# Performance work log

Measured on AMD Instinct MI355X. Metric: run time of the kernel, lower is better.

Reference implementation:

```python
import jax, jax.numpy as jnp
import numpy as np

B, S, D, H = 2, 4096, 768, 12
HD = D // H
SCALE = HD ** -0.5


def setup_inputs() -> dict:
    key = jax.random.key(0)
    k_x, k_wq, k_bq, k_wp, k_bp = jax.random.split(key, 5)
    lim_qkv = (1.0 / D) ** 0.5
    lim_p = (1.0 / D) ** 0.5
    return {
        "x": jax.random.normal(k_x, (B, S, D), dtype=jnp.float32),
        "qkv_w": jax.random.uniform(k_wq, (3 * D, D), dtype=jnp.float32, minval=-lim_qkv, maxval=lim_qkv),
        "qkv_b": jax.random.uniform(k_bq, (3 * D,), dtype=jnp.float32, minval=-lim_qkv, maxval=lim_qkv),
        "proj_w": jax.random.uniform(k_wp, (D, D), dtype=jnp.float32, minval=-lim_p, maxval=lim_p),
        "proj_b": jax.random.uniform(k_bp, (D,), dtype=jnp.float32, minval=-lim_p, maxval=lim_p),
    }


def reference(x, qkv_w, qkv_b, proj_w, proj_b):
    b, s, _ = x.shape
    qkv = x @ qkv_w.T + qkv_b                      # [b, s, 3D]
    q, k, v = jnp.split(qkv, 3, axis=-1)           # each [b, s, D]
    # [b, s, D] -> [b, H, s, HD]
    def to_heads(t):
        return t.reshape(b, s, H, HD).transpose(0, 2, 1, 3)
    q, k, v = to_heads(q), to_heads(k), to_heads(v)
    attn = jnp.einsum("bhqd,bhkd->bhqk", q, k) * SCALE   # [b, H, s, s]
    attn = jax.nn.softmax(attn, axis=-1)
    out = jnp.einsum("bhqk,bhkd->bhqd", attn, v)         # [b, H, s, HD]
    out = out.transpose(0, 2, 1, 3).reshape(b, s, D)
    return out @ proj_w.T + proj_b
```

## Files before the change

### kernel.cpp

```cpp
#include <hip/hip_runtime.h>
#include <hip/hip_bf16.h>


#define B_ 2
#define S_ 4096
#define D_ 768
#define H_ 12
#define HD_ 64
#define TD_ (3 * D_)
#define QKD_ (2 * D_)

static constexpr float LOG2E = 1.4426950408889634f;

typedef __bf16 bf16x8 __attribute__((ext_vector_type(8)));
typedef unsigned short ushortx8 __attribute__((ext_vector_type(8)));
typedef unsigned short ushortx4 __attribute__((ext_vector_type(4)));
typedef float floatx4 __attribute__((ext_vector_type(4)));

__device__ inline unsigned short f2bf(float f) {
  return __builtin_bit_cast(unsigned short, (__bf16)f);
}
__device__ inline float bf2f(unsigned short u) {
  return __uint_as_float(((unsigned int)u) << 16);
}
__device__ inline void glds16(const unsigned short* g, unsigned short* l) {
  __builtin_amdgcn_global_load_lds(
      (const __attribute__((address_space(1))) unsigned int*)g,
      (__attribute__((address_space(3))) unsigned int*)l, 16, 0, 0);
}

__global__ __launch_bounds__(256)
void cvt_bf16(const float* __restrict__ src, unsigned short* __restrict__ dst, int n4) {
  int idx = blockIdx.x * 256 + threadIdx.x;
  if (idx < n4) {
    floatx4 v = *reinterpret_cast<const floatx4*>(&src[(size_t)idx * 4]);
    ushortx4 o;
#pragma unroll
    for (int j = 0; j < 4; ++j) o[j] = f2bf(v[j]);
    *reinterpret_cast<ushortx4*>(&dst[(size_t)idx * 4]) = o;
  }
}

template <int NFR, bool QKV_EPI>
__global__ __launch_bounds__(256)
void gemm_bf16(const unsigned short* __restrict__ A,
               const unsigned short* __restrict__ W,
               const float* __restrict__ bias,
               float* __restrict__ Cf,
               unsigned short* __restrict__ qkbuf,
               unsigned short* __restrict__ vT,
               int M, int N, int K) {
  constexpr int BM = 128, BN = NFR * 32, BK = 64;
  __shared__ __attribute__((aligned(16))) unsigned short As[BM][BK];
  __shared__ __attribute__((aligned(16))) unsigned short Ws[BN][BK];

  const int tid = threadIdx.x;
  const int lane = tid & 63;
  const int wid = tid >> 6;
  const int wm = wid >> 1;
  const int wn = wid & 1;
  const int m0 = blockIdx.y * BM;
  const int n0 = blockIdx.x * BN;
  const int lr = lane & 15;
  const int g = lane >> 4;
  const int e8 = lr & 7;
  const int ro = g * 4;
  const int srow = lane >> 3;
  const int sch = lane & 7;

  floatx4 acc[4][NFR];
#pragma unroll
  for (int m = 0; m < 4; ++m)
#pragma unroll
    for (int n = 0; n < NFR; ++n) acc[m][n] = (floatx4){0.f, 0.f, 0.f, 0.f};

  for (int kb = 0; kb < K; kb += BK) {
#pragma unroll
    for (int c = 0; c < 4; ++c) {
      int seg = wid * 4 + c;
      int row = seg * 8 + srow;
      glds16(&A[(size_t)(m0 + row) * K + kb + ((sch ^ srow) << 3)], &As[seg * 8][0]);
    }
#pragma unroll
    for (int c = 0; c < NFR; ++c) {
      int seg = wid * NFR + c;
      int row = seg * 8 + srow;
      glds16(&W[(size_t)(n0 + row) * K + kb + ((sch ^ srow) << 3)], &Ws[seg * 8][0]);
    }
    __syncthreads();

#pragma unroll
    for (int ks = 0; ks < 2; ++ks) {
      int ch = ((ks << 2) + g) ^ e8;
      bf16x8 af[4], bfr[NFR];
#pragma unroll
      for (int m = 0; m < 4; ++m)
        af[m] = *reinterpret_cast<const bf16x8*>(&As[wm * 64 + m * 16 + lr][ch << 3]);
#pragma unroll
      for (int n = 0; n < NFR; ++n)
        bfr[n] = *reinterpret_cast<const bf16x8*>(&Ws[wn * (NFR * 16) + n * 16 + lr][ch << 3]);
#pragma unroll
      for (int m = 0; m < 4; ++m)
#pragma unroll
        for (int n = 0; n < NFR; ++n)
          acc[m][n] = __builtin_amdgcn_mfma_f32_16x16x32_bf16(af[m], bfr[n], acc[m][n], 0, 0, 0);
    }
    __syncthreads();
  }

#pragma unroll
  for (int n = 0; n < NFR; ++n) {
    int col = n0 + wn * (NFR * 16) + n * 16 + lr;
    float bv = bias[col];
#pragma unroll
    for (int m = 0; m < 4; ++m) {
      int row = m0 + wm * 64 + m * 16 + ro;
      if constexpr (QKV_EPI) {
        if (col >= QKD_) {
          int dcol = col - QKD_;
          int hh = dcol >> 6, dd = dcol & 63;
          int bb = row >> 12, s = row & (S_ - 1);
          int s5 = s & 31;
          int spos = (s & ~31) + ((s5 >> 2) & 3) * 8 + ((s5 >> 4) & 1) * 4;
          ushortx4 o4;
#pragma unroll
          for (int i = 0; i < 4; ++i) o4[i] = f2bf(acc[m][n][i] + bv);
          *reinterpret_cast<ushortx4*>(
              &vT[(size_t)((bb * H_ + hh) * 64 + dd) * S_ + spos]) = o4;
        } else {
#pragma unroll
          for (int i = 0; i < 4; ++i)
            qkbuf[(size_t)(row + i) * QKD_ + col] = f2bf(acc[m][n][i] + bv);
        }
      } else {
#pragma unroll
        for (int i = 0; i < 4; ++i)
          Cf[(size_t)(row + i) * N + col] = acc[m][n][i] + bv;
      }
    }
  }
}

template <int NSPLIT>
__global__ __launch_bounds__(256)
void attn_kernel(const unsigned short* __restrict__ qkbuf,
                 const unsigned short* __restrict__ vT,
                 unsigned short* __restrict__ outb,
                 float* __restrict__ po, float* __restrict__ pl) {
  constexpr int QB = 128, KVB = 64, NT = S_ / KVB / NSPLIT;
  __shared__ __attribute__((aligned(16))) unsigned short L[2 * 8192];

  const int tid = threadIdx.x;
  const int lane = tid & 63;
  const int wid = tid >> 6;
  const int q0 = blockIdx.x * QB;
  const int h = blockIdx.y;
  const int b = (NSPLIT == 1) ? blockIdx.z : (blockIdx.z >> 1);
  const int sp = (NSPLIT == 1) ? 0 : (blockIdx.z & 1);
  const int kvbase = sp * (S_ / NSPLIT);
  const int lr = lane & 15;
  const int g = lane >> 4;
  const int e8 = lr & 7;
  const int wq = wid * 32;

  const unsigned short* Qg = qkbuf + (size_t)b * S_ * QKD_ + (size_t)h * HD_;
  const unsigned short* Kg = Qg + D_;
  const unsigned short* Vg = vT + (size_t)(b * H_ + h) * HD_ * S_;

  const int srow = lane >> 3;
  const int sch = lane & 7;

  bf16x8 qf[2][2];
#pragma unroll
  for (int qt = 0; qt < 2; ++qt)
#pragma unroll
    for (int ks = 0; ks < 2; ++ks) {
      ushortx8 r = *reinterpret_cast<const ushortx8*>(
          &Qg[(size_t)(q0 + wq + qt * 16 + lr) * QKD_ + ks * 32 + g * 8]);
      bf16x8 q;
#pragma unroll
      for (int j = 0; j < 8; ++j) q[j] = (__bf16)(bf2f(r[j]) * (0.125f * LOG2E));
      qf[qt][ks] = q;
    }

  bf16x8 onesf;
#pragma unroll
  for (int j = 0; j < 8; ++j) onesf[j] = (__bf16)1.0f;

  floatx4 lacc[2] = {(floatx4){0.f, 0.f, 0.f, 0.f}, (floatx4){0.f, 0.f, 0.f, 0.f}};
  floatx4 oacc[2][4];
#pragma unroll
  for (int qt = 0; qt < 2; ++qt)
#pragma unroll
    for (int dt = 0; dt < 4; ++dt) oacc[qt][dt] = (floatx4){0.f, 0.f, 0.f, 0.f};

  int koff[4][2], voff[2][4];
#pragma unroll
  for (int kt = 0; kt < 4; ++kt)
#pragma unroll
    for (int ks = 0; ks < 2; ++ks)
      koff[kt][ks] = (kt * 16 + lr) * 64 + ((((ks << 2) + g) ^ e8) << 3);
#pragma unroll
  for (int ks = 0; ks < 2; ++ks)
#pragma unroll
    for (int dt = 0; dt < 4; ++dt)
      voff[ks][dt] = 4096 + (dt * 16 + lr) * 64 + ((((ks << 2) + g) ^ e8) << 3);

  const unsigned short* kp0 = Kg + (size_t)(kvbase + wid * 16 + srow) * QKD_ + ((sch ^ srow) << 3);
  const unsigned short* kp1 = kp0 + (size_t)8 * QKD_;
  const unsigned short* vp0 = Vg + (size_t)(wid * 16 + srow) * S_ + kvbase + ((sch ^ srow) << 3);
  const unsigned short* vp1 = vp0 + (size_t)8 * S_;

#define STAGE(BUF) do { \
    glds16(kp0, &L[(BUF) * 8192 + (wid * 16) * 64]); \
    glds16(kp1, &L[(BUF) * 8192 + (wid * 16 + 8) * 64]); \
    glds16(vp0, &L[(BUF) * 8192 + 4096 + (wid * 16) * 64]); \
    glds16(vp1, &L[(BUF) * 8192 + 4096 + (wid * 16 + 8) * 64]); \
    kp0 += (size_t)KVB * QKD_; kp1 += (size_t)KVB * QKD_; \
    vp0 += KVB; vp1 += KVB; } while (0)

#define COMPUTE(BUF) do { \
    bf16x8 kf[4][2], vf[2][4]; \
    _Pragma("unroll") \
    for (int kt = 0; kt < 4; ++kt) \
      _Pragma("unroll") \
      for (int ks = 0; ks < 2; ++ks) \
        kf[kt][ks] = *reinterpret_cast<const bf16x8*>(&L[(BUF) * 8192 + koff[kt][ks]]); \
    _Pragma("unroll") \
    for (int ks = 0; ks < 2; ++ks) \
      _Pragma("unroll") \
      for (int dt = 0; dt < 4; ++dt) \
        vf[ks][dt] = *reinterpret_cast<const bf16x8*>(&L[(BUF) * 8192 + voff[ks][dt]]); \
    _Pragma("unroll") \
    for (int qt = 0; qt < 2; ++qt) { \
      floatx4 sc[4]; \
      _Pragma("unroll") \
      for (int kt = 0; kt < 4; ++kt) { \
        floatx4 c = (floatx4){0.f, 0.f, 0.f, 0.f}; \
        _Pragma("unroll") \
        for (int ks = 0; ks < 2; ++ks) \
          c = __builtin_amdgcn_mfma_f32_16x16x32_bf16(kf[kt][ks], qf[qt][ks], c, 0, 0, 0); \
        sc[kt] = c; \
      } \
      _Pragma("unroll") \
      for (int kt = 0; kt < 4; ++kt) \
        _Pragma("unroll") \
        for (int i = 0; i < 4; ++i) \
          sc[kt][i] = __builtin_amdgcn_exp2f(sc[kt][i]); \
      bf16x8 pf0, pf1; \
      _Pragma("unroll") \
      for (int j = 0; j < 8; ++j) { \
        pf0[j] = (__bf16)sc[(j >> 2)][j & 3]; \
        pf1[j] = (__bf16)sc[2 + (j >> 2)][j & 3]; \
      } \
      lacc[qt] = __builtin_amdgcn_mfma_f32_16x16x32_bf16(onesf, pf0, lacc[qt], 0, 0, 0); \
      lacc[qt] = __builtin_amdgcn_mfma_f32_16x16x32_bf16(onesf, pf1, lacc[qt], 0, 0, 0); \
      _Pragma("unroll") \
      for (int dt = 0; dt < 4; ++dt) \
        oacc[qt][dt] = __builtin_amdgcn_mfma_f32_16x16x32_bf16(vf[0][dt], pf0, oacc[qt][dt], 0, 0, 0); \
      _Pragma("unroll") \
      for (int dt = 0; dt < 4; ++dt) \
        oacc[qt][dt] = __builtin_amdgcn_mfma_f32_16x16x32_bf16(vf[1][dt], pf1, oacc[qt][dt], 0, 0, 0); \
    } } while (0)

  STAGE(0);
  for (int t = 0; t < NT; t += 2) {
    __syncthreads();
    STAGE(1);
    COMPUTE(0);
    __syncthreads();
    if (t + 2 < NT) STAGE(0);
    COMPUTE(1);
  }
#undef STAGE
#undef COMPUTE

#pragma unroll
  for (int qt = 0; qt < 2; ++qt) {
    float l = lacc[qt][0];
    int q = q0 + wq + qt * 16 + lr;
    if constexpr (NSPLIT == 1) {
      float inv = __builtin_amdgcn_rcpf(l);
      size_t rowbase = ((size_t)b * S_ + q) * D_ + h * HD_;
#pragma unroll
      for (int dt = 0; dt < 4; ++dt) {
        ushortx4 o4;
#pragma unroll
        for (int i = 0; i < 4; ++i) o4[i] = f2bf(oacc[qt][dt][i] * inv);
        *reinterpret_cast<ushortx4*>(&outb[rowbase + dt * 16 + 4 * g]) = o4;
      }
    } else {
      size_t rowbase = ((size_t)(sp * B_ + b) * S_ + q) * D_ + h * HD_;
#pragma unroll
      for (int dt = 0; dt < 4; ++dt)
        *reinterpret_cast<floatx4*>(&po[rowbase + dt * 16 + 4 * g]) = oacc[qt][dt];
      if (lane < 16)
        pl[((size_t)((sp * B_ + b) * H_ + h)) * S_ + q] = l;
    }
  }
}

__global__ __launch_bounds__(256)
void combine_kernel(const float* __restrict__ po, const float* __restrict__ pl,
                    unsigned short* __restrict__ attnbuf) {
  int gid = blockIdx.x * 256 + threadIdx.x;
  int d4 = gid & 15;
  int rest = gid >> 4;
  int h = rest % H_;
  int bq = rest / H_;
  size_t o0 = (size_t)bq * D_ + h * 64 + d4 * 4;
  const size_t half = (size_t)B_ * S_ * D_;
  floatx4 a = *reinterpret_cast<const floatx4*>(&po[o0]);
  floatx4 c = *reinterpret_cast<const floatx4*>(&po[o0 + half]);
  int q = bq & (S_ - 1);
  int b = bq >> 12;
  float l = pl[(size_t)(b * H_ + h) * S_ + q] +
            pl[(size_t)((B_ + b) * H_ + h) * S_ + q];
  float inv = __builtin_amdgcn_rcpf(l);
  ushortx4 o;
#pragma unroll
  for (int i = 0; i < 4; ++i) o[i] = f2bf((a[i] + c[i]) * inv);
  *reinterpret_cast<ushortx4*>(&attnbuf[o0]) = o;
}

extern "C" void kernel_launch(void* const* d_in, const int* in_sizes, int n_in,
                              void* d_out, int out_size, void* d_ws, size_t ws_size,
                              hipStream_t stream) {
  const float* x      = (const float*)d_in[0];
  const float* qkv_w  = (const float*)d_in[1];
  const float* qkv_b  = (const float*)d_in[2];
  const float* proj_w = (const float*)d_in[3];
  const float* proj_b = (const float*)d_in[4];
  float* out = (float*)d_out;

  unsigned short* qkbuf   = (unsigned short*)d_ws;
  unsigned short* vTbuf   = qkbuf + (size_t)B_ * S_ * QKD_;
  unsigned short* attnbuf = vTbuf + (size_t)B_ * H_ * HD_ * S_;
  unsigned short* xbf     = attnbuf + (size_t)B_ * S_ * D_;
  unsigned short* wqkvbf  = xbf + (size_t)B_ * S_ * D_;
  unsigned short* wprojbf = wqkvbf + (size_t)TD_ * D_;
  float* po = (float*)(wprojbf + (size_t)D_ * D_);
  float* pl = po + (size_t)2 * B_ * S_ * D_;

  const size_t need = ((char*)(pl + (size_t)2 * B_ * H_ * S_)) - (char*)d_ws;
  const bool split = ws_size >= need;

  dim3 blk(256);
  cvt_bf16<<<dim3((B_ * S_ * D_ / 4 + 255) / 256), blk, 0, stream>>>(x, xbf, B_ * S_ * D_ / 4);
  cvt_bf16<<<dim3((TD_ * D_ / 4 + 255) / 256), blk, 0, stream>>>(qkv_w, wqkvbf, TD_ * D_ / 4);
  cvt_bf16<<<dim3((D_ * D_ / 4 + 255) / 256), blk, 0, stream>>>(proj_w, wprojbf, D_ * D_ / 4);

  gemm_bf16<4, true><<<dim3(TD_ / 128, (B_ * S_) / 128), blk, 0, stream>>>(
      xbf, wqkvbf, qkv_b, nullptr, qkbuf, vTbuf, B_ * S_, TD_, D_);

  if (split) {
    attn_kernel<2><<<dim3(S_ / 128, H_, B_ * 2), blk, 0, stream>>>(
        qkbuf, vTbuf, attnbuf, po, pl);
    combine_kernel<<<dim3(B_ * S_ * H_ * 16 / 256), blk, 0, stream>>>(po, pl, attnbuf);
  } else {
    attn_kernel<1><<<dim3(S_ / 128, H_, B_), blk, 0, stream>>>(
        qkbuf, vTbuf, attnbuf, nullptr, nullptr);
  }

  gemm_bf16<2, false><<<dim3(D_ / 64, (B_ * S_) / 128), blk, 0, stream>>>(
      attnbuf, wprojbf, proj_b, out, nullptr, nullptr, B_ * S_, D_, D_);
}
```

Baseline: 201.0 us.

## Drop split-KV attention with combine pass, fuse conversions, fold Q scale into GEMM

Removes the two-way KV split in attention and the combine kernel that merged the fp32 partial outputs and row sums. Every block now streams the full KV range and writes normalized bf16 output directly, which avoids the large fp32 partial-result round trip through memory. The cost is half as many attention blocks, so less parallelism to hide latency. It also merges the three fp32-to-bf16 conversion launches into one kernel and applies the softmax scale (times log2 e) to Q in the QKV GEMM epilogue, so the attention kernel no longer rescales Q when loading it.

After: 187.5 us, median of 3. 1.07x faster.

```diff
diff --git a/kernel.cpp b/kernel.cpp
--- a/kernel.cpp
+++ b/kernel.cpp
@@ -11,6 +11,7 @@
 #define QKD_ (2 * D_)
 
 static constexpr float LOG2E = 1.4426950408889634f;
+static constexpr float QSCL = 0.125f * LOG2E;
 
 typedef __bf16 bf16x8 __attribute__((ext_vector_type(8)));
 typedef unsigned short ushortx8 __attribute__((ext_vector_type(8)));
@@ -30,15 +31,20 @@
 }
 
 __global__ __launch_bounds__(256)
-void cvt_bf16(const float* __restrict__ src, unsigned short* __restrict__ dst, int n4) {
+void cvt_all(const float* __restrict__ s0, unsigned short* __restrict__ d0, int n0,
+             const float* __restrict__ s1, unsigned short* __restrict__ d1, int n1,
+             const float* __restrict__ s2, unsigned short* __restrict__ d2, int n2) {
   int idx = blockIdx.x * 256 + threadIdx.x;
-  if (idx < n4) {
-    floatx4 v = *reinterpret_cast<const floatx4*>(&src[(size_t)idx * 4]);
-    ushortx4 o;
-#pragma unroll
-    for (int j = 0; j < 4; ++j) o[j] = f2bf(v[j]);
-    *reinterpret_cast<ushortx4*>(&dst[(size_t)idx * 4]) = o;
-  }
+  const float* s; unsigned short* d;
+  if (idx < n0) { s = s0; d = d0; }
+  else if (idx < n0 + n1) { s = s1; d = d1; idx -= n0; }
+  else if (idx < n0 + n1 + n2) { s = s2; d = d2; idx -= n0 + n1; }
+  else return;
+  floatx4 v = *reinterpret_cast<const floatx4*>(&s[(size_t)idx * 4]);
+  ushortx4 o;
+#pragma unroll
+  for (int j = 0; j < 4; ++j) o[j] = f2bf(v[j]);
+  *reinterpret_cast<ushortx4*>(&d[(size_t)idx * 4]) = o;
 }
 
 template <int NFR, bool QKV_EPI>
@@ -128,9 +134,10 @@
           *reinterpret_cast<ushortx4*>(
               &vT[(size_t)((bb * H_ + hh) * 64 + dd) * S_ + spos]) = o4;
         } else {
+          const float scl = (col < D_) ? QSCL : 1.0f;
 #pragma unroll
           for (int i = 0; i < 4; ++i)
-            qkbuf[(size_t)(row + i) * QKD_ + col] = f2bf(acc[m][n][i] + bv);
+            qkbuf[(size_t)(row + i) * QKD_ + col] = f2bf((acc[m][n][i] + bv) * scl);
         }
       } else {
 #pragma unroll
@@ -141,13 +148,11 @@
   }
 }
 
-template <int NSPLIT>
 __global__ __launch_bounds__(256)
 void attn_kernel(const unsigned short* __restrict__ qkbuf,
                  const unsigned short* __restrict__ vT,
-                 unsigned short* __restrict__ outb,
-                 float* __restrict__ po, float* __restrict__ pl) {
-  constexpr int QB = 128, KVB = 64, NT = S_ / KVB / NSPLIT;
+                 unsigned short* __restrict__ outb) {
+  constexpr int QB = 128, KVB = 64, NT = S_ / KVB;
   __shared__ __attribute__((aligned(16))) unsigned short L[2 * 8192];
 
   const int tid = threadIdx.x;
@@ -155,9 +160,7 @@
   const int wid = tid >> 6;
   const int q0 = blockIdx.x * QB;
   const int h = blockIdx.y;
-  const int b = (NSPLIT == 1) ? blockIdx.z : (blockIdx.z >> 1);
-  const int sp = (NSPLIT == 1) ? 0 : (blockIdx.z & 1);
-  const int kvbase = sp * (S_ / NSPLIT);
+  const int b = blockIdx.z;
   const int lr = lane & 15;
   const int g = lane >> 4;
   const int e8 = lr & 7;
@@ -174,14 +177,9 @@
 #pragma unroll
   for (int qt = 0; qt < 2; ++qt)
 #pragma unroll
-    for (int ks = 0; ks < 2; ++ks) {
-      ushortx8 r = *reinterpret_cast<const ushortx8*>(
+    for (int ks = 0; ks < 2; ++ks)
+      qf[qt][ks] = *reinterpret_cast<const bf16x8*>(
           &Qg[(size_t)(q0 + wq + qt * 16 + lr) * QKD_ + ks * 32 + g * 8]);
-      bf16x8 q;
-#pragma unroll
-      for (int j = 0; j < 8; ++j) q[j] = (__bf16)(bf2f(r[j]) * (0.125f * LOG2E));
-      qf[qt][ks] = q;
-    }
 
   bf16x8 onesf;
 #pragma unroll
@@ -206,9 +204,9 @@
     for (int dt = 0; dt < 4; ++dt)
       voff[ks][dt] = 4096 + (dt * 16 + lr) * 64 + ((((ks << 2) + g) ^ e8) << 3);
 
-  const unsigned short* kp0 = Kg + (size_t)(kvbase + wid * 16 + srow) * QKD_ + ((sch ^ srow) << 3);
+  const unsigned short* kp0 = Kg + (size_t)(wid * 16 + srow) * QKD_ + ((sch ^ srow) << 3);
   const unsigned short* kp1 = kp0 + (size_t)8 * QKD_;
-  const unsigned short* vp0 = Vg + (size_t)(wid * 16 + srow) * S_ + kvbase + ((sch ^ srow) << 3);
+  const unsigned short* vp0 = Vg + (size_t)(wid * 16 + srow) * S_ + ((sch ^ srow) << 3);
   const unsigned short* vp1 = vp0 + (size_t)8 * S_;
 
 #define STAGE(BUF) do { \
@@ -279,48 +277,16 @@
   for (int qt = 0; qt < 2; ++qt) {
     float l = lacc[qt][0];
     int q = q0 + wq + qt * 16 + lr;
-    if constexpr (NSPLIT == 1) {
-      float inv = __builtin_amdgcn_rcpf(l);
-      size_t rowbase = ((size_t)b * S_ + q) * D_ + h * HD_;
-#pragma unroll
-      for (int dt = 0; dt < 4; ++dt) {
-        ushortx4 o4;
-#pragma unroll
-        for (int i = 0; i < 4; ++i) o4[i] = f2bf(oacc[qt][dt][i] * inv);
-        *reinterpret_cast<ushortx4*>(&outb[rowbase + dt * 16 + 4 * g]) = o4;
-      }
-    } else {
-      size_t rowbase = ((size_t)(sp * B_ + b) * S_ + q) * D_ + h * HD_;
-#pragma unroll
-      for (int dt = 0; dt < 4; ++dt)
-        *reinterpret_cast<floatx4*>(&po[rowbase + dt * 16 + 4 * g]) = oacc[qt][dt];
-      if (lane < 16)
-        pl[((size_t)((sp * B_ + b) * H_ + h)) * S_ + q] = l;
+    float inv = __builtin_amdgcn_rcpf(l);
+    size_t rowbase = ((size_t)b * S_ + q) * D_ + h * HD_;
+#pragma unroll
+    for (int dt = 0; dt < 4; ++dt) {
+      ushortx4 o4;
+#pragma unroll
+      for (int i = 0; i < 4; ++i) o4[i] = f2bf(oacc[qt][dt][i] * inv);
+      *reinterpret_cast<ushortx4*>(&outb[rowbase + dt * 16 + 4 * g]) = o4;
     }
   }
-}
-
-__global__ __launch_bounds__(256)
-void combine_kernel(const float* __restrict__ po, const float* __restrict__ pl,
-                    unsigned short* __restrict__ attnbuf) {
-  int gid = blockIdx.x * 256 + threadIdx.x;
-  int d4 = gid & 15;
-  int rest = gid >> 4;
-  int h = rest % H_;
-  int bq = rest / H_;
-  size_t o0 = (size_t)bq * D_ + h * 64 + d4 * 4;
-  const size_t half = (size_t)B_ * S_ * D_;
-  floatx4 a = *reinterpret_cast<const floatx4*>(&po[o0]);
-  floatx4 c = *reinterpret_cast<const floatx4*>(&po[o0 + half]);
-  int q = bq & (S_ - 1);
-  int b = bq >> 12;
-  float l = pl[(size_t)(b * H_ + h) * S_ + q] +
-            pl[(size_t)((B_ + b) * H_ + h) * S_ + q];
-  float inv = __builtin_amdgcn_rcpf(l);
-  ushortx4 o;
-#pragma unroll
-  for (int i = 0; i < 4; ++i) o[i] = f2bf((a[i] + c[i]) * inv);
-  *reinterpret_cast<ushortx4*>(&attnbuf[o0]) = o;
 }
 
 extern "C" void kernel_launch(void* const* d_in, const int* in_sizes, int n_in,
@@ -339,28 +305,16 @@
   unsigned short* xbf     = attnbuf + (size_t)B_ * S_ * D_;
   unsigned short* wqkvbf  = xbf + (size_t)B_ * S_ * D_;
   unsigned short* wprojbf = wqkvbf + (size_t)TD_ * D_;
-  float* po = (float*)(wprojbf + (size_t)D_ * D_);
-  float* pl = po + (size_t)2 * B_ * S_ * D_;
-
-  const size_t need = ((char*)(pl + (size_t)2 * B_ * H_ * S_)) - (char*)d_ws;
-  const bool split = ws_size >= need;
 
   dim3 blk(256);
-  cvt_bf16<<<dim3((B_ * S_ * D_ / 4 + 255) / 256), blk, 0, stream>>>(x, xbf, B_ * S_ * D_ / 4);
-  cvt_bf16<<<dim3((TD_ * D_ / 4 + 255) / 256), blk, 0, stream>>>(qkv_w, wqkvbf, TD_ * D_ / 4);
-  cvt_bf16<<<dim3((D_ * D_ / 4 + 255) / 256), blk, 0, stream>>>(proj_w, wprojbf, D_ * D_ / 4);
+  const int nx = B_ * S_ * D_ / 4, nw1 = TD_ * D_ / 4, nw2 = D_ * D_ / 4;
+  cvt_all<<<dim3((nx + nw1 + nw2 + 255) / 256), blk, 0, stream>>>(
+      x, xbf, nx, qkv_w, wqkvbf, nw1, proj_w, wprojbf, nw2);
 
   gemm_bf16<4, true><<<dim3(TD_ / 128, (B_ * S_) / 128), blk, 0, stream>>>(
       xbf, wqkvbf, qkv_b, nullptr, qkbuf, vTbuf, B_ * S_, TD_, D_);
 
-  if (split) {
-    attn_kernel<2><<<dim3(S_ / 128, H_, B_ * 2), blk, 0, stream>>>(
-        qkbuf, vTbuf, attnbuf, po, pl);
-    combine_kernel<<<dim3(B_ * S_ * H_ * 16 / 256), blk, 0, stream>>>(po, pl, attnbuf);
-  } else {
-    attn_kernel<1><<<dim3(S_ / 128, H_, B_), blk, 0, stream>>>(
-        qkbuf, vTbuf, attnbuf, nullptr, nullptr);
-  }
+  attn_kernel<<<dim3(S_ / 128, H_, B_), blk, 0, stream>>>(qkbuf, vTbuf, attnbuf);
 
   gemm_bf16<2, false><<<dim3(D_ / 64, (B_ * S_) / 128), blk, 0, stream>>>(
       attnbuf, wprojbf, proj_b, out, nullptr, nullptr, B_ * S_, D_, D_);
```
